# Kernel tuning notes

Measured on AMD Instinct MI355X. Metric: run time of the kernel, lower is better.

The kernel has to match this reference:

```python
import jax, jax.numpy as jnp
import numpy as np

NEG = jnp.float32(-1e30)  # log-semiring 'zero' (avoid -inf for safe grads)


def _ctc_total_scores(log_probs, targets, input_lengths, target_lengths):
    """Log-semiring forward over the composed CTC topology.

    log_probs: (T, N, C) log-softmax outputs, blank id = 0
    targets:   (N*L,) flat labels in [1, C)
    Returns tot_scores (N,): log p(targets | log_probs) per utterance,
    identical to k2.intersect_dense + get_tot_scores(log_semiring=True).
    """
    T, N, C = log_probs.shape
    L = targets.shape[0] // N
    tgt = targets.reshape(N, L).astype(jnp.int32)
    S = 2 * L + 1  # extended sequence: blank y1 blank y2 ... yL blank

    ext = jnp.zeros((N, S), jnp.int32).at[:, 1::2].set(tgt)
    s_idx = jnp.arange(S)
    # skip transition s-2 -> s allowed only for label states with ext[s] != ext[s-2]
    diff = jnp.concatenate([jnp.zeros((N, 2), bool), ext[:, 2:] != ext[:, :-2]], axis=1)
    skip_ok = (s_idx[None, :] % 2 == 1) & (s_idx[None, :] >= 2) & diff
    # states beyond this utterance's extended length are invalid
    valid = s_idx[None, :] <= 2 * target_lengths.astype(jnp.int32)[:, None]
    s_end = 2 * target_lengths.astype(jnp.int32)  # index of final blank state

    def emit(lp):  # (N, C) -> (N, S): gather log-probs of extended labels
        return jnp.take_along_axis(lp, ext, axis=1)

    e0 = emit(log_probs[0])
    a0 = jnp.full((N, S), NEG).at[:, 0].set(e0[:, 0]).at[:, 1].set(e0[:, 1])
    a0 = jnp.where(valid, a0, NEG)

    def final_score(a):  # logsumexp over the two accepting states
        last = jnp.take_along_axis(a, s_end[:, None], axis=1)[:, 0]
        prev = jnp.take_along_axis(a, (s_end - 1)[:, None], axis=1)[:, 0]
        return jnp.logaddexp(last, prev)

    def step(a, lp):
        sh1 = jnp.concatenate([jnp.full((N, 1), NEG), a[:, :-1]], axis=1)
        sh2 = jnp.concatenate([jnp.full((N, 2), NEG), a[:, :-2]], axis=1)
        sh2 = jnp.where(skip_ok, sh2, NEG)
        a_new = jnp.logaddexp(jnp.logaddexp(a, sh1), sh2) + emit(lp)
        a_new = jnp.where(valid, a_new, NEG)
        return a_new, final_score(a_new)

    _, finals = jax.lax.scan(step, a0, log_probs[1:])  # finals: (T-1, N)
    finals = jnp.concatenate([final_score(a0)[None], finals], axis=0)  # (T, N)
    tot = jnp.take_along_axis(finals, (input_lengths.astype(jnp.int32) - 1)[None, :], axis=0)[0]
    return tot


def setup_inputs() -> dict:
    key = jax.random.key(0)
    k1, k2_ = jax.random.split(key)
    T, N, C, L = 1500, 32, 1024, 100
    log_probs = jax.nn.log_softmax(
        jax.random.normal(k1, (T, N, C), dtype=jnp.float32), axis=-1)
    targets = jax.random.randint(k2_, (N * L,), 1, C, dtype=jnp.int32)  # no blanks
    input_lengths = jnp.full((N,), T, dtype=jnp.int32)
    target_lengths = jnp.full((N,), L, dtype=jnp.int32)
    return {"log_probs": log_probs, "targets": targets,
            "input_lengths": input_lengths, "target_lengths": target_lengths}


def reference(log_probs, targets, input_lengths, target_lengths):
    tot = _ctc_total_scores(log_probs, targets, input_lengths, target_lengths)
    # drop -inf (failed) segments like get_tot_objf_and_num_frames, then negate sum
    finite = tot > jnp.float32(-1e29)
    return -jnp.sum(jnp.where(finite, tot, 0.0))
```

## Files before the change

### kernel.cpp

```cpp
#include <hip/hip_runtime.h>
#include <stdint.h>

#define NEGF  (-1e30f)
#define LOG2E 1.4426950408889634f
#define LN2F  0.6931471805599453f

__device__ __forceinline__ float fexp2(float x) {
#if __has_builtin(__builtin_amdgcn_exp2f)
    return __builtin_amdgcn_exp2f(x);
#else
    return exp2f(x);
#endif
}
__device__ __forceinline__ float flog2(float x) {
#if __has_builtin(__builtin_amdgcn_logf)
    return __builtin_amdgcn_logf(x);
#else
    return log2f(x);
#endif
}
__device__ __forceinline__ float lse2(float a, float b) {
    float m  = fmaxf(a, b);
    float mn = fminf(a, b);
    return m + flog2(1.0f + fexp2(mn - m));
}
__device__ __forceinline__ float lse3(float a, float b, float c) {
    float m = fmaxf(fmaxf(a, b), c);
    float s = fexp2(a - m) + fexp2(b - m) + fexp2(c - m);
    return m + flog2(s);
}

#define RB  16
#define VMW "s_waitcnt vmcnt(56)"

__device__ __forceinline__ void stage_row(const float* __restrict__ src, float* dst)
{
    const int lane = threadIdx.x;
    const float* g = src + (lane << 2);
    __builtin_amdgcn_global_load_lds((const __attribute__((address_space(1))) void*)(g),
        (__attribute__((address_space(3))) void*)(dst), 16, 0, 0);
    __builtin_amdgcn_global_load_lds((const __attribute__((address_space(1))) void*)(g + 256),
        (__attribute__((address_space(3))) void*)(dst + 256), 16, 0, 0);
    __builtin_amdgcn_global_load_lds((const __attribute__((address_space(1))) void*)(g + 512),
        (__attribute__((address_space(3))) void*)(dst + 512), 16, 0, 0);
    __builtin_amdgcn_global_load_lds((const __attribute__((address_space(1))) void*)(g + 768),
        (__attribute__((address_space(3))) void*)(dst + 768), 16, 0, 0);
}

__device__ __forceinline__ void lds_read3(uint32_t sb, uint32_t o1, uint32_t o3,
                                          float& eb, float& e1, float& e3)
{
    asm volatile("s_mov_b32 m0, -1\n\t"
                 "ds_read_b32 %0, %3\n\t"
                 "ds_read_b32 %1, %4\n\t"
                 "ds_read_b32 %2, %5"
                 : "=&v"(eb), "=&v"(e1), "=&v"(e3)
                 : "v"(sb), "v"(sb + o1), "v"(sb + o3)
                 : "memory");
}
__device__ __forceinline__ void lds_read4(uint32_t sb, uint32_t o1, uint32_t o3, uint32_t o5,
                                          float& eb, float& e1, float& e3, float& e5)
{
    asm volatile("s_mov_b32 m0, -1\n\t"
                 "ds_read_b32 %0, %4\n\t"
                 "ds_read_b32 %1, %5\n\t"
                 "ds_read_b32 %2, %6\n\t"
                 "ds_read_b32 %3, %7"
                 : "=&v"(eb), "=&v"(e1), "=&v"(e3), "=&v"(e5)
                 : "v"(sb), "v"(sb + o1), "v"(sb + o3), "v"(sb + o5)
                 : "memory");
}

__global__ __launch_bounds__(64, 1)
void ctc_scan(const float* __restrict__ lp, const int* __restrict__ tgt,
              const int* __restrict__ ilen, const int* __restrict__ tlen,
              float* __restrict__ wsA, float* __restrict__ wsB,
              int T, int N, int C, int L)
{
    __shared__ float ring[RB * 1024];

    const int  b      = blockIdx.x;
    const bool is_fwd = (b < N);
    const int  n      = is_fwd ? b : (b - N);
    const int  lane   = threadIdx.x;
    const int  len_t  = tlen[n];
    const int  len_in = ilen[n];
    const int  tm     = (len_in - 1) >> 1;
    const int  send   = 2 * len_t;

    const long tb = (long)n * L;
    auto getT = [&](int k) -> int {
        return (k >= 0 && k < len_t) ? tgt[tb + k] : 0;
    };
    const int lm1 = getT(2 * lane - 1);
    const int l1  = getT(2 * lane);
    const int l2  = getT(2 * lane + 1);
    const int l3  = getT(2 * lane + 2);
    const uint32_t o1 = (uint32_t)l1 << 2;
    const uint32_t o3 = (uint32_t)l2 << 2;
    const uint32_t o5 = (uint32_t)l3 << 2;
    const bool skip1 = (lane > 0) && (l1 != lm1);
    const bool skip3 = (l2 != l1);
    const bool skip5 = (l3 != l2);
    const int  s0 = 4 * lane;
    const bool v0 = (s0     <= send);
    const bool v1 = (s0 + 1 <= send);
    const bool v2 = (s0 + 2 <= send);
    const bool v3 = (s0 + 3 <= send);

    const long   rstride = (long)N * C;
    const float* row0    = lp + (long)n * C;
    const uint32_t ringb =
        (uint32_t)(uintptr_t)(const __attribute__((address_space(3))) void*)ring;

    if (is_fwd) {
        float eb0 = row0[0];
        float e10 = row0[l1];
        float a0 = (lane == 0) ? eb0 * LOG2E : NEGF;
        float a1 = (lane == 0 && 1 <= send) ? e10 * LOG2E : NEGF;
        float a2 = NEGF, a3 = NEGF;
        float p3 = __shfl_up(a3, 1, 64);

        const int nsteps = tm;
        const int lim    = len_in - 1;
        for (int j = 0; j < RB - 1; ++j) {
            int r = 1 + j; if (r > lim) r = lim;
            stage_row(row0 + (long)r * rstride, ring + (j << 10));
        }
        asm volatile(VMW ::: "memory");
        float eb, e1, e3;
        lds_read3(ringb, o1, o3, eb, e1, e3);

        for (int i = 0; i < nsteps; ++i) {
            int r = i + RB; if (r > lim) r = lim;
            stage_row(row0 + (long)r * rstride,
                      ring + (((i + RB - 1) & (RB - 1)) << 10));
            asm volatile("s_waitcnt lgkmcnt(0)" ::: "memory");
            __builtin_amdgcn_sched_barrier(0);
            {
                float ebl = eb * LOG2E, e1l = e1 * LOG2E, e3l = e3 * LOG2E;
                float pm = (lane == 0) ? NEGF : p3;
                float n0 = lse2(a0, pm) + ebl;
                float n1 = lse3(a1, a0, skip1 ? pm : NEGF) + e1l;
                float n2 = lse2(a2, a1) + ebl;
                float n3 = lse3(a3, a2, skip3 ? a1 : NEGF) + e3l;
                a0 = v0 ? n0 : NEGF;
                a1 = v1 ? n1 : NEGF;
                a2 = v2 ? n2 : NEGF;
                a3 = v3 ? n3 : NEGF;
                p3 = __shfl_up(a3, 1, 64);
            }
            asm volatile(VMW ::: "memory");
            uint32_t sb = ringb + (uint32_t)(((i + 1) & (RB - 1)) << 12);
            lds_read3(sb, o1, o3, eb, e1, e3);
        }
        asm volatile("s_waitcnt vmcnt(0) lgkmcnt(0)" ::: "memory");
        *((float4*)(wsA + (long)n * 256) + lane) = make_float4(a0, a1, a2, a3);
    } else {
        float b0 = (s0     == send || s0     == send - 1) ? 0.0f : NEGF;
        float b1 = (s0 + 1 == send || s0 + 1 == send - 1) ? 0.0f : NEGF;
        float b2 = (s0 + 2 == send || s0 + 2 == send - 1) ? 0.0f : NEGF;
        float b3 = (s0 + 3 == send || s0 + 3 == send - 1) ? 0.0f : NEGF;
        b0 = v0 ? b0 : NEGF; b1 = v1 ? b1 : NEGF;
        b2 = v2 ? b2 : NEGF; b3 = v3 ? b3 : NEGF;
        float q0 = __shfl_down(b0, 1, 64);
        float q1 = __shfl_down(b1, 1, 64);

        const int nsteps = len_in - 1 - tm;
        for (int j = 0; j < RB - 1; ++j) {
            int r = len_in - 1 - j; if (r < 0) r = 0;
            stage_row(row0 + (long)r * rstride, ring + (j << 10));
        }
        asm volatile(VMW ::: "memory");
        float eb, e1, e3, e5;
        lds_read4(ringb, o1, o3, o5, eb, e1, e3, e5);

        for (int i = 0; i < nsteps; ++i) {
            int r = len_in - 1 - (i + RB - 1); if (r < 0) r = 0;
            stage_row(row0 + (long)r * rstride,
                      ring + (((i + RB - 1) & (RB - 1)) << 10));
            asm volatile("s_waitcnt lgkmcnt(0)" ::: "memory");
            __builtin_amdgcn_sched_barrier(0);
            {
                float ebl = eb * LOG2E, e1l = e1 * LOG2E;
                float e3l = e3 * LOG2E, e5l = e5 * LOG2E;
                float f0 = b0 + ebl;
                float f1 = b1 + e1l;
                float f2 = b2 + ebl;
                float f3 = b3 + e3l;
                float f0p = (lane == 63) ? NEGF : (q0 + ebl);
                float f1p = (lane == 63) ? NEGF : (q1 + e5l);
                float n0 = lse2(f0, f1);
                float n1 = lse3(f1, f2, skip3 ? f3 : NEGF);
                float n2 = lse2(f2, f3);
                float n3 = lse3(f3, f0p, skip5 ? f1p : NEGF);
                b0 = v0 ? n0 : NEGF;
                b1 = v1 ? n1 : NEGF;
                b2 = v2 ? n2 : NEGF;
                b3 = v3 ? n3 : NEGF;
                q0 = __shfl_down(b0, 1, 64);
                q1 = __shfl_down(b1, 1, 64);
            }
            asm volatile(VMW ::: "memory");
            uint32_t sb = ringb + (uint32_t)(((i + 1) & (RB - 1)) << 12);
            lds_read4(sb, o1, o3, o5, eb, e1, e3, e5);
        }
        asm volatile("s_waitcnt vmcnt(0) lgkmcnt(0)" ::: "memory");
        *((float4*)(wsB + (long)n * 256) + lane) = make_float4(b0, b1, b2, b3);
    }
}

__global__ __launch_bounds__(64, 1)
void ctc_combine(const float* __restrict__ wsA, const float* __restrict__ wsB,
                 float* __restrict__ out)
{
    const int n = blockIdx.x;
    const int lane = threadIdx.x;
    const float4 A = *((const float4*)(wsA + (long)n * 256) + lane);
    const float4 B = *((const float4*)(wsB + (long)n * 256) + lane);
    float v = lse2(lse2(A.x + B.x, A.y + B.y), lse2(A.z + B.z, A.w + B.w));
    #pragma unroll
    for (int off = 1; off < 64; off <<= 1) {
        float o = __shfl_xor(v, off, 64);
        v = lse2(v, o);
    }
    if (lane == 0) {
        float tot = v * LN2F;
        if (tot > -1e29f) atomicAdd(out, -tot);
    }
}

extern "C" void kernel_launch(void* const* d_in, const int* in_sizes, int n_in,
                              void* d_out, int out_size, void* d_ws, size_t ws_size,
                              hipStream_t stream) {
    const float* lp      = (const float*)d_in[0];
    const int*   targets = (const int*)d_in[1];
    const int*   in_len  = (const int*)d_in[2];
    const int*   tgt_len = (const int*)d_in[3];
    const int N = in_sizes[2];
    const int L = in_sizes[1] / N;
    const int C = 1024;
    const int T = (int)((long)in_sizes[0] / ((long)N * C));

    float* out = (float*)d_out;
    float* wsA = (float*)d_ws;
    float* wsB = wsA + (long)N * 256;

    hipMemsetAsync(out, 0, sizeof(float), stream);
    ctc_scan<<<2 * N, 64, 0, stream>>>(lp, targets, in_len, tgt_len,
                                       wsA, wsB, T, N, C, L);
    ctc_combine<<<N, 64, 0, stream>>>(wsA, wsB, out);
}
```

Measured before the change: 352.9 us.

## Double-buffer LDS emission reads and use DPP lane shifts in CTC scan

Unrolls the forward and backward recurrences by two and keeps two register sets of emission values in flight. The LDS reads for the next step now overlap the current step, gated by partial lgkmcnt waits instead of a full drain. Cross-lane shuffles are replaced with DPP row shifts that fill with NEG, and the per-state validity selects are dropped. Risks: DPP row_shr/shl only moves data within 16-lane rows, so values may not cross row boundaries correctly; removing the validity masks may also change results for shorter targets.

Measured after the change: 336.6 us. 1.05x faster.

```diff
diff --git a/kernel.cpp b/kernel.cpp
--- a/kernel.cpp
+++ b/kernel.cpp
@@ -30,8 +30,19 @@
     return m + flog2(s);
 }
 
+__device__ __forceinline__ float dpp_shr1(float x, float fill) {
+    int r = __builtin_amdgcn_update_dpp(__float_as_int(fill), __float_as_int(x),
+                                        0x138, 0xf, 0xf, false);
+    return __int_as_float(r);
+}
+__device__ __forceinline__ float dpp_shl1(float x, float fill) {
+    int r = __builtin_amdgcn_update_dpp(__float_as_int(fill), __float_as_int(x),
+                                        0x130, 0xf, 0xf, false);
+    return __int_as_float(r);
+}
+
 #define RB  16
-#define VMW "s_waitcnt vmcnt(56)"
+#define VMW "s_waitcnt vmcnt(52)"
 
 __device__ __forceinline__ void stage_row(const float* __restrict__ src, float* dst)
 {
@@ -70,6 +81,11 @@
                  : "v"(sb), "v"(sb + o1), "v"(sb + o3), "v"(sb + o5)
                  : "memory");
 }
+
+#define LGKM_WAIT3(c, x0, x1, x2) \
+    asm volatile("s_waitcnt lgkmcnt(" #c ")" : "+v"(x0), "+v"(x1), "+v"(x2) :: "memory")
+#define LGKM_WAIT4(c, x0, x1, x2, x3) \
+    asm volatile("s_waitcnt lgkmcnt(" #c ")" : "+v"(x0), "+v"(x1), "+v"(x2), "+v"(x3) :: "memory")
 
 __global__ __launch_bounds__(64, 1)
 void ctc_scan(const float* __restrict__ lp, const int* __restrict__ tgt,
@@ -103,23 +119,31 @@
     const bool skip3 = (l2 != l1);
     const bool skip5 = (l3 != l2);
     const int  s0 = 4 * lane;
-    const bool v0 = (s0     <= send);
-    const bool v1 = (s0 + 1 <= send);
-    const bool v2 = (s0 + 2 <= send);
-    const bool v3 = (s0 + 3 <= send);
 
     const long   rstride = (long)N * C;
     const float* row0    = lp + (long)n * C;
     const uint32_t ringb =
         (uint32_t)(uintptr_t)(const __attribute__((address_space(3))) void*)ring;
 
+
     if (is_fwd) {
         float eb0 = row0[0];
         float e10 = row0[l1];
+        asm volatile("s_waitcnt vmcnt(0)" : "+v"(eb0), "+v"(e10) :: "memory");
         float a0 = (lane == 0) ? eb0 * LOG2E : NEGF;
         float a1 = (lane == 0 && 1 <= send) ? e10 * LOG2E : NEGF;
         float a2 = NEGF, a3 = NEGF;
-        float p3 = __shfl_up(a3, 1, 64);
+        float p3 = NEGF;
+
+        auto fstep = [&](float ebr, float e1r, float e3r) {
+            float eb = ebr * LOG2E, e1 = e1r * LOG2E, e3 = e3r * LOG2E;
+            float n0 = lse2(a0, p3) + eb;
+            float n1 = lse3(a1, a0, skip1 ? p3 : NEGF) + e1;
+            float n2 = lse2(a2, a1) + eb;
+            float n3 = lse3(a3, a2, skip3 ? a1 : NEGF) + e3;
+            a0 = n0; a1 = n1; a2 = n2; a3 = n3;
+            p3 = dpp_shr1(a3, NEGF);
+        };
 
         const int nsteps = tm;
         const int lim    = len_in - 1;
@@ -128,31 +152,31 @@
             stage_row(row0 + (long)r * rstride, ring + (j << 10));
         }
         asm volatile(VMW ::: "memory");
-        float eb, e1, e3;
-        lds_read3(ringb, o1, o3, eb, e1, e3);
-
-        for (int i = 0; i < nsteps; ++i) {
-            int r = i + RB; if (r > lim) r = lim;
-            stage_row(row0 + (long)r * rstride,
-                      ring + (((i + RB - 1) & (RB - 1)) << 10));
-            asm volatile("s_waitcnt lgkmcnt(0)" ::: "memory");
-            __builtin_amdgcn_sched_barrier(0);
-            {
-                float ebl = eb * LOG2E, e1l = e1 * LOG2E, e3l = e3 * LOG2E;
-                float pm = (lane == 0) ? NEGF : p3;
-                float n0 = lse2(a0, pm) + ebl;
-                float n1 = lse3(a1, a0, skip1 ? pm : NEGF) + e1l;
-                float n2 = lse2(a2, a1) + ebl;
-                float n3 = lse3(a3, a2, skip3 ? a1 : NEGF) + e3l;
-                a0 = v0 ? n0 : NEGF;
-                a1 = v1 ? n1 : NEGF;
-                a2 = v2 ? n2 : NEGF;
-                a3 = v3 ? n3 : NEGF;
-                p3 = __shfl_up(a3, 1, 64);
-            }
-            asm volatile(VMW ::: "memory");
-            uint32_t sb = ringb + (uint32_t)(((i + 1) & (RB - 1)) << 12);
-            lds_read3(sb, o1, o3, eb, e1, e3);
+        float ebA, e1A, e3A, ebB, e1B, e3B;
+        lds_read3(ringb,        o1, o3, ebA, e1A, e3A);
+        lds_read3(ringb + 4096, o1, o3, ebB, e1B, e3B);
+
+        int i = 0;
+        for (; i + 1 < nsteps; i += 2) {
+            {   int s = i + RB - 1; int r = s + 1; if (r > lim) r = lim;
+                stage_row(row0 + (long)r * rstride, ring + ((s & (RB - 1)) << 10)); }
+            LGKM_WAIT3(3, ebA, e1A, e3A);
+            fstep(ebA, e1A, e3A);
+            asm volatile(VMW ::: "memory");
+            lds_read3(ringb + (uint32_t)(((i + 2) & (RB - 1)) << 12), o1, o3,
+                      ebA, e1A, e3A);
+
+            {   int s = i + RB; int r = s + 1; if (r > lim) r = lim;
+                stage_row(row0 + (long)r * rstride, ring + ((s & (RB - 1)) << 10)); }
+            LGKM_WAIT3(3, ebB, e1B, e3B);
+            fstep(ebB, e1B, e3B);
+            asm volatile(VMW ::: "memory");
+            lds_read3(ringb + (uint32_t)(((i + 3) & (RB - 1)) << 12), o1, o3,
+                      ebB, e1B, e3B);
+        }
+        if (i < nsteps) {
+            LGKM_WAIT3(0, ebA, e1A, e3A);
+            fstep(ebA, e1A, e3A);
         }
         asm volatile("s_waitcnt vmcnt(0) lgkmcnt(0)" ::: "memory");
         *((float4*)(wsA + (long)n * 256) + lane) = make_float4(a0, a1, a2, a3);
@@ -161,49 +185,58 @@
         float b1 = (s0 + 1 == send || s0 + 1 == send - 1) ? 0.0f : NEGF;
         float b2 = (s0 + 2 == send || s0 + 2 == send - 1) ? 0.0f : NEGF;
         float b3 = (s0 + 3 == send || s0 + 3 == send - 1) ? 0.0f : NEGF;
-        b0 = v0 ? b0 : NEGF; b1 = v1 ? b1 : NEGF;
-        b2 = v2 ? b2 : NEGF; b3 = v3 ? b3 : NEGF;
-        float q0 = __shfl_down(b0, 1, 64);
-        float q1 = __shfl_down(b1, 1, 64);
+        float q0 = dpp_shl1(b0, NEGF);
+        float q1 = dpp_shl1(b1, NEGF);
+
+        auto bstep = [&](float ebr, float e1r, float e3r, float e5r) {
+            float ebl = ebr * LOG2E, e1l = e1r * LOG2E;
+            float e3l = e3r * LOG2E, e5l = e5r * LOG2E;
+            float f0 = b0 + ebl;
+            float f1 = b1 + e1l;
+            float f2 = b2 + ebl;
+            float f3 = b3 + e3l;
+            float f0p = q0 + ebl;
+            float f1p = q1 + e5l;
+            b0 = lse2(f0, f1);
+            b1 = lse3(f1, f2, skip3 ? f3 : NEGF);
+            b2 = lse2(f2, f3);
+            b3 = lse3(f3, f0p, skip5 ? f1p : NEGF);
+            q0 = dpp_shl1(b0, NEGF);
+            q1 = dpp_shl1(b1, NEGF);
+        };
 
         const int nsteps = len_in - 1 - tm;
+        asm volatile("s_waitcnt vmcnt(0)" ::: "memory");
         for (int j = 0; j < RB - 1; ++j) {
             int r = len_in - 1 - j; if (r < 0) r = 0;
             stage_row(row0 + (long)r * rstride, ring + (j << 10));
         }
         asm volatile(VMW ::: "memory");
-        float eb, e1, e3, e5;
-        lds_read4(ringb, o1, o3, o5, eb, e1, e3, e5);
-
-        for (int i = 0; i < nsteps; ++i) {
-            int r = len_in - 1 - (i + RB - 1); if (r < 0) r = 0;
-            stage_row(row0 + (long)r * rstride,
-                      ring + (((i + RB - 1) & (RB - 1)) << 10));
-            asm volatile("s_waitcnt lgkmcnt(0)" ::: "memory");
-            __builtin_amdgcn_sched_barrier(0);
-            {
-                float ebl = eb * LOG2E, e1l = e1 * LOG2E;
-                float e3l = e3 * LOG2E, e5l = e5 * LOG2E;
-                float f0 = b0 + ebl;
-                float f1 = b1 + e1l;
-                float f2 = b2 + ebl;
-                float f3 = b3 + e3l;
-                float f0p = (lane == 63) ? NEGF : (q0 + ebl);
-                float f1p = (lane == 63) ? NEGF : (q1 + e5l);
-                float n0 = lse2(f0, f1);
-                float n1 = lse3(f1, f2, skip3 ? f3 : NEGF);
-                float n2 = lse2(f2, f3);
-                float n3 = lse3(f3, f0p, skip5 ? f1p : NEGF);
-                b0 = v0 ? n0 : NEGF;
-                b1 = v1 ? n1 : NEGF;
-                b2 = v2 ? n2 : NEGF;
-                b3 = v3 ? n3 : NEGF;
-                q0 = __shfl_down(b0, 1, 64);
-                q1 = __shfl_down(b1, 1, 64);
-            }
-            asm volatile(VMW ::: "memory");
-            uint32_t sb = ringb + (uint32_t)(((i + 1) & (RB - 1)) << 12);
-            lds_read4(sb, o1, o3, o5, eb, e1, e3, e5);
+        float ebA, e1A, e3A, e5A, ebB, e1B, e3B, e5B;
+        lds_read4(ringb,        o1, o3, o5, ebA, e1A, e3A, e5A);
+        lds_read4(ringb + 4096, o1, o3, o5, ebB, e1B, e3B, e5B);
+
+        int i = 0;
+        for (; i + 1 < nsteps; i += 2) {
+            {   int s = i + RB - 1; int r = len_in - 1 - s; if (r < 0) r = 0;
+                stage_row(row0 + (long)r * rstride, ring + ((s & (RB - 1)) << 10)); }
+            LGKM_WAIT4(4, ebA, e1A, e3A, e5A);
+            bstep(ebA, e1A, e3A, e5A);
+            asm volatile(VMW ::: "memory");
+            lds_read4(ringb + (uint32_t)(((i + 2) & (RB - 1)) << 12), o1, o3, o5,
+                      ebA, e1A, e3A, e5A);
+
+            {   int s = i + RB; int r = len_in - 1 - s; if (r < 0) r = 0;
+                stage_row(row0 + (long)r * rstride, ring + ((s & (RB - 1)) << 10)); }
+            LGKM_WAIT4(4, ebB, e1B, e3B, e5B);
+            bstep(ebB, e1B, e3B, e5B);
+            asm volatile(VMW ::: "memory");
+            lds_read4(ringb + (uint32_t)(((i + 3) & (RB - 1)) << 12), o1, o3, o5,
+                      ebB, e1B, e3B, e5B);
+        }
+        if (i < nsteps) {
+            LGKM_WAIT4(0, ebA, e1A, e3A, e5A);
+            bstep(ebA, e1A, e3A, e5A);
         }
         asm volatile("s_waitcnt vmcnt(0) lgkmcnt(0)" ::: "memory");
         *((float4*)(wsB + (long)n * 256) + lane) = make_float4(b0, b1, b2, b3);
```
